# Optimization experiments

Hardware: AMD Instinct MI355X
Metric: run time of the kernel (lower is better)

## Reference

```python
import jax, jax.numpy as jnp
import numpy as np

NUM_TILES = 64
TPC = 8            # tiles per cluster
GRID = 16          # spline grid size
EPS = 1e-5


def setup_inputs() -> dict:
    key = jax.random.key(0)
    ks = jax.random.split(key, 6)
    B, S, D, T, DH, G = 2, 1024, 512, NUM_TILES, 128, GRID
    x = jax.random.normal(ks[0], (B, S, D), dtype=jnp.float32)
    gamma = jnp.ones((D,), jnp.float32)
    beta = jnp.zeros((D,), jnp.float32)
    # torch layouts: down.weight [DH, D], up.weight [D, DH]
    Wd = jax.random.normal(ks[1], (T, DH, D), dtype=jnp.float32) * 0.02
    spline_bases = jax.random.normal(ks[2], (T, DH, G), dtype=jnp.float32) * 0.1
    spline_slopes = jax.random.normal(ks[3], (T, DH, G), dtype=jnp.float32) * 0.1
    Wu = jax.random.normal(ks[4], (T, D, DH), dtype=jnp.float32) * 0.02
    scale = jnp.full((T,), 0.1, jnp.float32)
    return {"x": x, "gamma": gamma, "beta": beta, "Wd": Wd,
            "spline_bases": spline_bases, "spline_slopes": spline_slopes,
            "Wu": Wu, "scale": scale}


def reference(x, gamma, beta, Wd, spline_bases, spline_slopes, Wu, scale):
    B, S, D = x.shape
    T, DH, _ = Wd.shape
    C = T // TPC
    N = B * S

    # LayerNorm
    mu = x.mean(-1, keepdims=True)
    var = ((x - mu) ** 2).mean(-1, keepdims=True)
    xn = (x - mu) * jax.lax.rsqrt(var + EPS) * gamma + beta
    xf = xn.reshape(N, D)

    # Signatures (first call: ema == current tile signatures)
    tile_sigs = jnp.sign(Wd.mean(axis=1))                         # [T, D]
    cluster_sigs = jnp.sign(tile_sigs.reshape(C, TPC, D).mean(1))  # [C, D]

    # Hierarchical routing: cluster -> tile
    in_sigs = jnp.sign(xf)                                        # [N, D]
    best_c = jnp.argmax(in_sigs @ cluster_sigs.T, axis=-1)        # [N]
    tile_scores = (in_sigs @ tile_sigs.T).reshape(N, C, TPC)      # [N, C, TPC]
    sc = jnp.take_along_axis(tile_scores, best_c[:, None, None], axis=1)[:, 0, :]
    local_best = jnp.argmax(sc, axis=-1)                          # [N]
    tidx = best_c * TPC + local_best                              # [N]

    # Dispatch: gather per-token expert weights, down-project
    h = jnp.einsum('nd,nhd->nh', xf, Wd[tidx])                    # [N, DH]

    # Spline nonlinearity
    hn = jax.nn.sigmoid(h)
    idx = jnp.clip((hn * GRID).astype(jnp.int32), 0, GRID - 1)    # [N, DH]
    base = jnp.take_along_axis(spline_bases[tidx], idx[..., None], axis=-1)[..., 0]
    slope = jnp.take_along_axis(spline_slopes[tidx], idx[..., None], axis=-1)[..., 0]
    local_pos = hn * GRID - idx.astype(h.dtype)                   # (hn - idx*cell)/cell
    hs = base + slope * local_pos                                 # [N, DH]

    # Up-project, per-tile scale, combine (dropout is identity in eval)
    y = jnp.einsum('nh,ndh->nd', hs, Wu[tidx]) * scale[tidx][:, None]
    return x + y.reshape(B, S, D)
```

## Files before the change

### kernel.cpp

```cpp
#include <hip/hip_runtime.h>
#include <hip/hip_bf16.h>
#include <math.h>

#define NTILES 64
#define TPC 8
#define NCLUST 8
#define GRID_SZ 16
#define DIM 512
#define DHID 128
#define NTOK 2048
#define LN_EPS 1e-5f
#define TB 16
#define NCHUNK_MAX 192

typedef __attribute__((ext_vector_type(8))) short bf16x8;
typedef __attribute__((ext_vector_type(4))) float f32x4;

static __device__ __forceinline__ float fsign(float v) {
    return (v > 0.f) ? 1.f : ((v < 0.f) ? -1.f : 0.f);
}

static __device__ __forceinline__ unsigned short bf16bits(float f) {
    union { __hip_bfloat16 h; unsigned short s; } u;
    u.h = __float2bfloat16(f);
    return u.s;
}

static __device__ __forceinline__ bf16x8 cvt8(const float* p) {
    float4 a = *(const float4*)p;
    float4 b = *(const float4*)(p + 4);
    float e[8] = {a.x, a.y, a.z, a.w, b.x, b.y, b.z, b.w};
    bf16x8 v;
    #pragma unroll
    for (int i = 0; i < 8; ++i) v[i] = (short)bf16bits(e[i]);
    return v;
}

static __device__ __forceinline__ bool route_chunk(const int* counts, int lane, int cb,
                                                   int& t, int& base, int& m) {
    int cnt_l = counts[lane];
    int nck = (cnt_l + TB - 1) / TB;
    int pre = nck;
    #pragma unroll
    for (int off = 1; off < 64; off <<= 1) {
        int u = __shfl_up(pre, off);
        if (lane >= off) pre += u;
    }
    int total = __shfl(pre, 63);
    pre -= nck;
    if (cb >= total) return false;
    unsigned long long msk = __ballot(cb >= pre && cb < pre + nck);
    t = (int)__builtin_ctzll(msk);
    base = (cb - __shfl(pre, t)) * TB;
    m = min(TB, __shfl(cnt_l, t) - base);
    return true;
}

__global__ __launch_bounds__(256) void k_prep(const float* __restrict__ x,
                                              const float* __restrict__ gamma,
                                              const float* __restrict__ beta,
                                              const float* __restrict__ Wd,
                                              const float* __restrict__ Wu,
                                              float* __restrict__ psum,
                                              unsigned short* __restrict__ wd_b,
                                              unsigned short* __restrict__ wu_b,
                                              unsigned short* __restrict__ xn_b,
                                              int* __restrict__ counts) {
    int bid = blockIdx.x;
    int tid = threadIdx.x;
    if (bid < 512) {
        int t = bid >> 3, part = bid & 7;
        const float* basep = Wd + ((size_t)t * DHID + part * 16) * DIM;
        unsigned short* bb = wd_b + ((size_t)t * DHID + part * 16) * DIM;
        #pragma unroll
        for (int k2 = 0; k2 < 2; ++k2) {
            int d = tid + k2 * 256;
            float s = 0.f;
            #pragma unroll
            for (int j = 0; j < 16; ++j) {
                float v = basep[(size_t)j * DIM + d];
                s += v;
                bb[(size_t)j * DIM + d] = bf16bits(v);
            }
            psum[((size_t)t * 8 + part) * DIM + d] = s;
        }
        if (bid == 0 && tid < NTILES) counts[tid] = 0;
    } else if (bid < 1024) {
        int n = (bid - 512) * 4 + (tid >> 6);
        int lane = tid & 63;
        const float* xr = x + (size_t)n * DIM;
        float v[8];
        float sum = 0.f;
        #pragma unroll
        for (int j = 0; j < 8; ++j) { float t = xr[lane + 64 * j]; v[j] = t; sum += t; }
        #pragma unroll
        for (int off = 32; off; off >>= 1) sum += __shfl_xor(sum, off);
        float mu = sum * (1.f / DIM);
        float sq = 0.f;
        #pragma unroll
        for (int j = 0; j < 8; ++j) { float t = v[j] - mu; sq += t * t; }
        #pragma unroll
        for (int off = 32; off; off >>= 1) sq += __shfl_xor(sq, off);
        float rs = rsqrtf(sq * (1.f / DIM) + LN_EPS);
        #pragma unroll
        for (int j = 0; j < 8; ++j) {
            int d = lane + 64 * j;
            float xv = (v[j] - mu) * rs * gamma[d] + beta[d];
            xn_b[(size_t)n * DIM + d] = bf16bits(xv);
        }
    } else {
        size_t basei = (size_t)(bid - 1024) * 8192;
        #pragma unroll
        for (int k = 0; k < 4; ++k) {
            size_t off = basei + (size_t)tid * 8 + (size_t)k * 2048;
            bf16x8 v = cvt8(Wu + off);
            *(bf16x8*)(wu_b + off) = v;
        }
    }
}

__global__ __launch_bounds__(512) void k_csig(const float* __restrict__ psum,
                                              float* __restrict__ tile_sigs,
                                              float* __restrict__ cluster_sigs) {
    int c = blockIdx.x, d = threadIdx.x;
    float csum = 0.f;
    #pragma unroll
    for (int k = 0; k < TPC; ++k) {
        int t = c * TPC + k;
        float s = 0.f;
        #pragma unroll
        for (int p = 0; p < 8; ++p) s += psum[((size_t)t * 8 + p) * DIM + d];
        float sg = fsign(s);
        tile_sigs[(size_t)t * DIM + d] = sg;
        csum += sg;
    }
    cluster_sigs[(size_t)c * DIM + d] = fsign(csum);
}

__global__ __launch_bounds__(256) void k_route(const unsigned short* __restrict__ xn_b,
                                               const float* __restrict__ tile_sigs,
                                               const float* __restrict__ cluster_sigs,
                                               int* __restrict__ counts,
                                               int* __restrict__ list) {
    int n = blockIdx.x * 4 + (threadIdx.x >> 6);
    int lane = threadIdx.x & 63;
    float sg[8];
    #pragma unroll
    for (int j = 0; j < 8; ++j) {
        unsigned short u = xn_b[(size_t)n * DIM + lane + 64 * j];
        sg[j] = ((u & 0x7fff) == 0) ? 0.f : ((u & 0x8000) ? -1.f : 1.f);
    }
    int best_c = 0; float best = -1e30f;
    for (int c = 0; c < NCLUST; ++c) {
        float s = 0.f;
        #pragma unroll
        for (int j = 0; j < 8; ++j) s += sg[j] * cluster_sigs[(size_t)c * DIM + lane + 64 * j];
        #pragma unroll
        for (int off = 32; off; off >>= 1) s += __shfl_xor(s, off);
        if (s > best) { best = s; best_c = c; }
    }
    int bt = best_c * TPC; float bts = -1e30f;
    for (int k = 0; k < TPC; ++k) {
        int t = best_c * TPC + k;
        float s = 0.f;
        #pragma unroll
        for (int j = 0; j < 8; ++j) s += sg[j] * tile_sigs[(size_t)t * DIM + lane + 64 * j];
        #pragma unroll
        for (int off = 32; off; off >>= 1) s += __shfl_xor(s, off);
        if (s > bts) { bts = s; bt = t; }
    }
    if (lane == 0) {
        int slot = atomicAdd(&counts[bt], 1);
        list[(size_t)bt * NTOK + slot] = n;
    }
}

__global__ __launch_bounds__(512, 2) void k_ffn(const float* __restrict__ x,
                                                const unsigned short* __restrict__ xn_b,
                                                const unsigned short* __restrict__ wd_b,
                                                const float* __restrict__ sb,
                                                const float* __restrict__ ss,
                                                const unsigned short* __restrict__ wu_b,
                                                const float* __restrict__ scale,
                                                const int* __restrict__ counts,
                                                const int* __restrict__ list,
                                                float* __restrict__ out) {
    int tid = threadIdx.x;
    int lane = tid & 63;
    int wv = tid >> 6;
    int cb = ((int)blockIdx.x & 7) * (NCHUNK_MAX / 8) + ((int)blockIdx.x >> 3);
    int t, base, m;
    if (!route_chunk(counts, lane, cb, t, base, m)) return;

    __shared__ __align__(16) unsigned short hsl[TB * DHID];

    int mrow = lane & 15;
    int ko = (lane >> 4) * 8;
    int tokm = list[(size_t)t * NTOK + base + min(mrow, m - 1)];

    const unsigned short* xr = xn_b + (size_t)tokm * DIM;
    const unsigned short* wr = wd_b + ((size_t)t * DHID + wv * 16 + mrow) * DIM;
    f32x4 acc = {0.f, 0.f, 0.f, 0.f};
    #pragma unroll
    for (int kk = 0; kk < 16; ++kk) {
        int d = kk * 32 + ko;
        bf16x8 a = *(const bf16x8*)(xr + d);
        bf16x8 b = *(const bf16x8*)(wr + d);
        acc = __builtin_amdgcn_mfma_f32_16x16x32_bf16(a, b, acc, 0, 0, 0);
    }
    int dh = wv * 16 + mrow;
    const float* sbt = sb + ((size_t)t * DHID + dh) * GRID_SZ;
    const float* sst = ss + ((size_t)t * DHID + dh) * GRID_SZ;
    #pragma unroll
    for (int r = 0; r < 4; ++r) {
        int tr = (lane >> 4) * 4 + r;
        float h = acc[r];
        float hn = 1.f / (1.f + expf(-h));
        float g = hn * (float)GRID_SZ;
        int idx = (int)g;
        idx = idx > GRID_SZ - 1 ? GRID_SZ - 1 : idx;
        float lp = g - (float)idx;
        float val = sbt[idx] + sst[idx] * lp;
        hsl[(tr * DHID + dh) ^ ((tr & 7) << 3)] = bf16bits(val);
    }
    __syncthreads();

    float sc_t = scale[t];
    bf16x8 a2[4];
    #pragma unroll
    for (int kk = 0; kk < 4; ++kk)
        a2[kk] = *(const bf16x8*)&hsl[(mrow * DHID + kk * 32 + ko) ^ ((mrow & 7) << 3)];
    #pragma unroll
    for (int nt = 0; nt < 4; ++nt) {
        int d = wv * 64 + nt * 16 + mrow;
        const unsigned short* wru = wu_b + ((size_t)t * DIM + d) * DHID;
        f32x4 au = {0.f, 0.f, 0.f, 0.f};
        #pragma unroll
        for (int kk = 0; kk < 4; ++kk) {
            bf16x8 b = *(const bf16x8*)(wru + kk * 32 + ko);
            au = __builtin_amdgcn_mfma_f32_16x16x32_bf16(a2[kk], b, au, 0, 0, 0);
        }
        #pragma unroll
        for (int r = 0; r < 4; ++r) {
            int tr = (lane >> 4) * 4 + r;
            int tok_tr = __shfl(tokm, tr);
            if (tr < m) {
                size_t o = (size_t)tok_tr * DIM + d;
                out[o] = x[o] + au[r] * sc_t;
            }
        }
    }
}

extern "C" void kernel_launch(void* const* d_in, const int* in_sizes, int n_in,
                              void* d_out, int out_size, void* d_ws, size_t ws_size,
                              hipStream_t stream) {
    const float* x     = (const float*)d_in[0];
    const float* gamma = (const float*)d_in[1];
    const float* beta  = (const float*)d_in[2];
    const float* Wd    = (const float*)d_in[3];
    const float* sb    = (const float*)d_in[4];
    const float* ss    = (const float*)d_in[5];
    const float* Wu    = (const float*)d_in[6];
    const float* scale = (const float*)d_in[7];
    float* out = (float*)d_out;

    float* psum          = (float*)d_ws;
    float* tile_sigs     = psum + (size_t)NTILES * 8 * DIM;
    float* cluster_sigs  = tile_sigs + NTILES * DIM;
    int*   counts        = (int*)(cluster_sigs + NCLUST * DIM);
    int*   list          = counts + NTILES;
    unsigned short* xn_b = (unsigned short*)(list + (size_t)NTILES * NTOK);
    unsigned short* wd_b = xn_b + (size_t)NTOK * DIM;
    unsigned short* wu_b = wd_b + (size_t)NTILES * DHID * DIM;

    k_prep<<<1536, 256, 0, stream>>>(x, gamma, beta, Wd, Wu, psum, wd_b, wu_b, xn_b, counts);
    k_csig<<<NCLUST, 512, 0, stream>>>(psum, tile_sigs, cluster_sigs);
    k_route<<<NTOK / 4, 256, 0, stream>>>(xn_b, tile_sigs, cluster_sigs, counts, list);
    k_ffn<<<NCHUNK_MAX, 512, 0, stream>>>(x, xn_b, wd_b, sb, ss, wu_b, scale, counts, list, out);
}
```

Measured before the change: 51.94 us.

## Fuse four kernels into one persistent kernel with global atomic flag barriers

Replaces the prep, signature, routing and FFN launches with a single 1024-block kernel. Stages are ordered with global atomic counters and spin-waits instead of kernel boundaries, removing launch gaps and tail idle time. The FFN stage now uses 256-thread blocks that each cover two hidden and output slices per wave, and the Wu conversion is folded into the LayerNorm blocks. This depends on all 1024 blocks being co-resident, since otherwise the spin-waits deadlock, and it adds a memset and atomic polling traffic.

```diff
diff --git a/kernel.cpp b/kernel.cpp
--- a/kernel.cpp
+++ b/kernel.cpp
@@ -12,6 +12,12 @@
 #define LN_EPS 1e-5f
 #define TB 16
 #define NCHUNK_MAX 192
+#define NBLK 1024
+
+#define FA1 0
+#define FA2 16
+#define FB  32
+#define FC  48
 
 typedef __attribute__((ext_vector_type(8))) short bf16x8;
 typedef __attribute__((ext_vector_type(4))) float f32x4;
@@ -36,40 +42,35 @@
     return v;
 }
 
-static __device__ __forceinline__ bool route_chunk(const int* counts, int lane, int cb,
-                                                   int& t, int& base, int& m) {
-    int cnt_l = counts[lane];
-    int nck = (cnt_l + TB - 1) / TB;
-    int pre = nck;
-    #pragma unroll
-    for (int off = 1; off < 64; off <<= 1) {
-        int u = __shfl_up(pre, off);
-        if (lane >= off) pre += u;
-    }
-    int total = __shfl(pre, 63);
-    pre -= nck;
-    if (cb >= total) return false;
-    unsigned long long msk = __ballot(cb >= pre && cb < pre + nck);
-    t = (int)__builtin_ctzll(msk);
-    base = (cb - __shfl(pre, t)) * TB;
-    m = min(TB, __shfl(cnt_l, t) - base);
-    return true;
-}
-
-__global__ __launch_bounds__(256) void k_prep(const float* __restrict__ x,
-                                              const float* __restrict__ gamma,
-                                              const float* __restrict__ beta,
-                                              const float* __restrict__ Wd,
-                                              const float* __restrict__ Wu,
-                                              float* __restrict__ psum,
-                                              unsigned short* __restrict__ wd_b,
-                                              unsigned short* __restrict__ wu_b,
-                                              unsigned short* __restrict__ xn_b,
-                                              int* __restrict__ counts) {
-    int bid = blockIdx.x;
+static __device__ __forceinline__ void wait_flag(int* f, int target) {
+    while (atomicAdd(f, 0) < target) __builtin_amdgcn_s_sleep(8);
+}
+
+__global__ __launch_bounds__(256, 4) void k_all(const float* __restrict__ x,
+                                                const float* __restrict__ gamma,
+                                                const float* __restrict__ beta,
+                                                const float* __restrict__ Wd,
+                                                const float* __restrict__ sb,
+                                                const float* __restrict__ ss,
+                                                const float* __restrict__ Wu,
+                                                const float* __restrict__ scale,
+                                                float* __restrict__ out,
+                                                int* __restrict__ flags,
+                                                float* __restrict__ psum,
+                                                float* __restrict__ tile_sigs,
+                                                float* __restrict__ cluster_sigs,
+                                                int* __restrict__ counts,
+                                                int* __restrict__ list,
+                                                unsigned short* __restrict__ xn_b,
+                                                unsigned short* __restrict__ wd_b,
+                                                unsigned short* __restrict__ wu_b) {
+    int b = blockIdx.x;
     int tid = threadIdx.x;
-    if (bid < 512) {
-        int t = bid >> 3, part = bid & 7;
+    int lane = tid & 63;
+    int wv = tid >> 6;
+
+    if (b < 512) {
+        int t = b >> 3, part = b & 7;
         const float* basep = Wd + ((size_t)t * DHID + part * 16) * DIM;
         unsigned short* bb = wd_b + ((size_t)t * DHID + part * 16) * DIM;
         #pragma unroll
@@ -84,10 +85,8 @@
             }
             psum[((size_t)t * 8 + part) * DIM + d] = s;
         }
-        if (bid == 0 && tid < NTILES) counts[tid] = 0;
-    } else if (bid < 1024) {
-        int n = (bid - 512) * 4 + (tid >> 6);
-        int lane = tid & 63;
+    } else {
+        int n = (b - 512) * 4 + wv;
         const float* xr = x + (size_t)n * DIM;
         float v[8];
         float sum = 0.f;
@@ -108,120 +107,143 @@
             float xv = (v[j] - mu) * rs * gamma[d] + beta[d];
             xn_b[(size_t)n * DIM + d] = bf16bits(xv);
         }
-    } else {
-        size_t basei = (size_t)(bid - 1024) * 8192;
+        size_t basei = (size_t)(b - 512) * 8192;
         #pragma unroll
         for (int k = 0; k < 4; ++k) {
             size_t off = basei + (size_t)tid * 8 + (size_t)k * 2048;
-            bf16x8 v = cvt8(Wu + off);
-            *(bf16x8*)(wu_b + off) = v;
-        }
-    }
-}
-
-__global__ __launch_bounds__(512) void k_csig(const float* __restrict__ psum,
-                                              float* __restrict__ tile_sigs,
-                                              float* __restrict__ cluster_sigs) {
-    int c = blockIdx.x, d = threadIdx.x;
-    float csum = 0.f;
-    #pragma unroll
-    for (int k = 0; k < TPC; ++k) {
-        int t = c * TPC + k;
-        float s = 0.f;
-        #pragma unroll
-        for (int p = 0; p < 8; ++p) s += psum[((size_t)t * 8 + p) * DIM + d];
-        float sg = fsign(s);
-        tile_sigs[(size_t)t * DIM + d] = sg;
-        csum += sg;
-    }
-    cluster_sigs[(size_t)c * DIM + d] = fsign(csum);
-}
-
-__global__ __launch_bounds__(256) void k_route(const unsigned short* __restrict__ xn_b,
-                                               const float* __restrict__ tile_sigs,
-                                               const float* __restrict__ cluster_sigs,
-                                               int* __restrict__ counts,
-                                               int* __restrict__ list) {
-    int n = blockIdx.x * 4 + (threadIdx.x >> 6);
-    int lane = threadIdx.x & 63;
-    float sg[8];
-    #pragma unroll
-    for (int j = 0; j < 8; ++j) {
-        unsigned short u = xn_b[(size_t)n * DIM + lane + 64 * j];
-        sg[j] = ((u & 0x7fff) == 0) ? 0.f : ((u & 0x8000) ? -1.f : 1.f);
-    }
-    int best_c = 0; float best = -1e30f;
-    for (int c = 0; c < NCLUST; ++c) {
-        float s = 0.f;
-        #pragma unroll
-        for (int j = 0; j < 8; ++j) s += sg[j] * cluster_sigs[(size_t)c * DIM + lane + 64 * j];
-        #pragma unroll
-        for (int off = 32; off; off >>= 1) s += __shfl_xor(s, off);
-        if (s > best) { best = s; best_c = c; }
-    }
-    int bt = best_c * TPC; float bts = -1e30f;
-    for (int k = 0; k < TPC; ++k) {
-        int t = best_c * TPC + k;
-        float s = 0.f;
-        #pragma unroll
-        for (int j = 0; j < 8; ++j) s += sg[j] * tile_sigs[(size_t)t * DIM + lane + 64 * j];
-        #pragma unroll
-        for (int off = 32; off; off >>= 1) s += __shfl_xor(s, off);
-        if (s > bts) { bts = s; bt = t; }
-    }
-    if (lane == 0) {
-        int slot = atomicAdd(&counts[bt], 1);
-        list[(size_t)bt * NTOK + slot] = n;
-    }
-}
-
-__global__ __launch_bounds__(512, 2) void k_ffn(const float* __restrict__ x,
-                                                const unsigned short* __restrict__ xn_b,
-                                                const unsigned short* __restrict__ wd_b,
-                                                const float* __restrict__ sb,
-                                                const float* __restrict__ ss,
-                                                const unsigned short* __restrict__ wu_b,
-                                                const float* __restrict__ scale,
-                                                const int* __restrict__ counts,
-                                                const int* __restrict__ list,
-                                                float* __restrict__ out) {
-    int tid = threadIdx.x;
-    int lane = tid & 63;
-    int wv = tid >> 6;
-    int cb = ((int)blockIdx.x & 7) * (NCHUNK_MAX / 8) + ((int)blockIdx.x >> 3);
+            *(bf16x8*)(wu_b + off) = cvt8(Wu + off);
+        }
+    }
+    __syncthreads();
+    if (tid == 0) {
+        __threadfence();
+        atomicAdd(&flags[b < 512 ? FA1 : FA2], 1);
+    }
+    if (b >= 512) return;
+
+    if (b < NCLUST) {
+        if (tid == 0) { wait_flag(&flags[FA1], 512); __threadfence(); }
+        __syncthreads();
+        if (tid < TPC) counts[b * TPC + tid] = 0;
+        #pragma unroll
+        for (int k2 = 0; k2 < 2; ++k2) {
+            int d = tid + k2 * 256;
+            float csum = 0.f;
+            #pragma unroll
+            for (int k = 0; k < TPC; ++k) {
+                int t = b * TPC + k;
+                float s = 0.f;
+                #pragma unroll
+                for (int p = 0; p < 8; ++p) s += psum[((size_t)t * 8 + p) * DIM + d];
+                float sg = fsign(s);
+                tile_sigs[(size_t)t * DIM + d] = sg;
+                csum += sg;
+            }
+            cluster_sigs[(size_t)b * DIM + d] = fsign(csum);
+        }
+        __syncthreads();
+        if (tid == 0) { __threadfence(); atomicAdd(&flags[FB], 1); }
+    }
+
+    if (tid == 0) {
+        wait_flag(&flags[FB], NCLUST);
+        wait_flag(&flags[FA2], 512);
+        __threadfence();
+    }
+    __syncthreads();
+    {
+        int n = b * 4 + wv;
+        float sg[8];
+        #pragma unroll
+        for (int j = 0; j < 8; ++j) {
+            unsigned short u = xn_b[(size_t)n * DIM + lane + 64 * j];
+            sg[j] = ((u & 0x7fff) == 0) ? 0.f : ((u & 0x8000) ? -1.f : 1.f);
+        }
+        int best_c = 0; float best = -1e30f;
+        for (int c = 0; c < NCLUST; ++c) {
+            float s = 0.f;
+            #pragma unroll
+            for (int j = 0; j < 8; ++j) s += sg[j] * cluster_sigs[(size_t)c * DIM + lane + 64 * j];
+            #pragma unroll
+            for (int off = 32; off; off >>= 1) s += __shfl_xor(s, off);
+            if (s > best) { best = s; best_c = c; }
+        }
+        int bt = best_c * TPC; float bts = -1e30f;
+        for (int k = 0; k < TPC; ++k) {
+            int t = best_c * TPC + k;
+            float s = 0.f;
+            #pragma unroll
+            for (int j = 0; j < 8; ++j) s += sg[j] * tile_sigs[(size_t)t * DIM + lane + 64 * j];
+            #pragma unroll
+            for (int off = 32; off; off >>= 1) s += __shfl_xor(s, off);
+            if (s > bts) { bts = s; bt = t; }
+        }
+        if (lane == 0) {
+            int slot = atomicAdd(&counts[bt], 1);
+            list[(size_t)bt * NTOK + slot] = n;
+        }
+    }
+    __syncthreads();
+    if (tid == 0) { __threadfence(); atomicAdd(&flags[FC], 1); }
+    if (b >= NCHUNK_MAX) return;
+
+    if (tid == 0) { wait_flag(&flags[FC], 512); __threadfence(); }
+    __syncthreads();
+
+    int cb = (b & 7) * (NCHUNK_MAX / 8) + (b >> 3);
     int t, base, m;
-    if (!route_chunk(counts, lane, cb, t, base, m)) return;
+    {
+        int cnt_l = atomicAdd(&counts[lane], 0);
+        int nck = (cnt_l + TB - 1) / TB;
+        int pre = nck;
+        #pragma unroll
+        for (int off = 1; off < 64; off <<= 1) {
+            int u = __shfl_up(pre, off);
+            if (lane >= off) pre += u;
+        }
+        int total = __shfl(pre, 63);
+        pre -= nck;
+        if (cb >= total) return;
+        unsigned long long msk = __ballot(cb >= pre && cb < pre + nck);
+        t = (int)__builtin_ctzll(msk);
+        base = (cb - __shfl(pre, t)) * TB;
+        m = min(TB, __shfl(cnt_l, t) - base);
+    }
 
     __shared__ __align__(16) unsigned short hsl[TB * DHID];
 
     int mrow = lane & 15;
     int ko = (lane >> 4) * 8;
     int tokm = list[(size_t)t * NTOK + base + min(mrow, m - 1)];
-
     const unsigned short* xr = xn_b + (size_t)tokm * DIM;
-    const unsigned short* wr = wd_b + ((size_t)t * DHID + wv * 16 + mrow) * DIM;
-    f32x4 acc = {0.f, 0.f, 0.f, 0.f};
+
     #pragma unroll
-    for (int kk = 0; kk < 16; ++kk) {
-        int d = kk * 32 + ko;
-        bf16x8 a = *(const bf16x8*)(xr + d);
-        bf16x8 b = *(const bf16x8*)(wr + d);
-        acc = __builtin_amdgcn_mfma_f32_16x16x32_bf16(a, b, acc, 0, 0, 0);
-    }
-    int dh = wv * 16 + mrow;
-    const float* sbt = sb + ((size_t)t * DHID + dh) * GRID_SZ;
-    const float* sst = ss + ((size_t)t * DHID + dh) * GRID_SZ;
-    #pragma unroll
-    for (int r = 0; r < 4; ++r) {
-        int tr = (lane >> 4) * 4 + r;
-        float h = acc[r];
-        float hn = 1.f / (1.f + expf(-h));
-        float g = hn * (float)GRID_SZ;
-        int idx = (int)g;
-        idx = idx > GRID_SZ - 1 ? GRID_SZ - 1 : idx;
-        float lp = g - (float)idx;
-        float val = sbt[idx] + sst[idx] * lp;
-        hsl[(tr * DHID + dh) ^ ((tr & 7) << 3)] = bf16bits(val);
+    for (int j = 0; j < 2; ++j) {
+        int dtile = wv + j * 4;
+        const unsigned short* wr = wd_b + ((size_t)t * DHID + dtile * 16 + mrow) * DIM;
+        f32x4 acc = {0.f, 0.f, 0.f, 0.f};
+        #pragma unroll
+        for (int kk = 0; kk < 16; ++kk) {
+            int d = kk * 32 + ko;
+            bf16x8 a = *(const bf16x8*)(xr + d);
+            bf16x8 w = *(const bf16x8*)(wr + d);
+            acc = __builtin_amdgcn_mfma_f32_16x16x32_bf16(a, w, acc, 0, 0, 0);
+        }
+        int dh = dtile * 16 + mrow;
+        const float* sbt = sb + ((size_t)t * DHID + dh) * GRID_SZ;
+        const float* sst = ss + ((size_t)t * DHID + dh) * GRID_SZ;
+        #pragma unroll
+        for (int r = 0; r < 4; ++r) {
+            int tr = (lane >> 4) * 4 + r;
+            float h = acc[r];
+            float hn = 1.f / (1.f + expf(-h));
+            float g = hn * (float)GRID_SZ;
+            int idx = (int)g;
+            idx = idx > GRID_SZ - 1 ? GRID_SZ - 1 : idx;
+            float lp = g - (float)idx;
+            float val = sbt[idx] + sst[idx] * lp;
+            hsl[(tr * DHID + dh) ^ ((tr & 7) << 3)] = bf16bits(val);
+        }
     }
     __syncthreads();
 
@@ -231,22 +253,26 @@
     for (int kk = 0; kk < 4; ++kk)
         a2[kk] = *(const bf16x8*)&hsl[(mrow * DHID + kk * 32 + ko) ^ ((mrow & 7) << 3)];
     #pragma unroll
-    for (int nt = 0; nt < 4; ++nt) {
-        int d = wv * 64 + nt * 16 + mrow;
-        const unsigned short* wru = wu_b + ((size_t)t * DIM + d) * DHID;
-        f32x4 au = {0.f, 0.f, 0.f, 0.f};
-        #pragma unroll
-        for (int kk = 0; kk < 4; ++kk) {
-            bf16x8 b = *(const bf16x8*)(wru + kk * 32 + ko);
-            au = __builtin_amdgcn_mfma_f32_16x16x32_bf16(a2[kk], b, au, 0, 0, 0);
-        }
-        #pragma unroll
-        for (int r = 0; r < 4; ++r) {
-            int tr = (lane >> 4) * 4 + r;
-            int tok_tr = __shfl(tokm, tr);
-            if (tr < m) {
-                size_t o = (size_t)tok_tr * DIM + d;
-                out[o] = x[o] + au[r] * sc_t;
+    for (int j = 0; j < 2; ++j) {
+        int sl = wv + j * 4;
+        #pragma unroll
+        for (int nt = 0; nt < 4; ++nt) {
+            int d = sl * 64 + nt * 16 + mrow;
+            const unsigned short* wru = wu_b + ((size_t)t * DIM + d) * DHID;
+            f32x4 au = {0.f, 0.f, 0.f, 0.f};
+            #pragma unroll
+            for (int kk = 0; kk < 4; ++kk) {
+                bf16x8 w = *(const bf16x8*)(wru + kk * 32 + ko);
+                au = __builtin_amdgcn_mfma_f32_16x16x32_bf16(a2[kk], w, au, 0, 0, 0);
+            }
+            #pragma unroll
+            for (int r = 0; r < 4; ++r) {
+                int tr = (lane >> 4) * 4 + r;
+                int tok_tr = __shfl(tokm, tr);
+                if (tr < m) {
+                    size_t o = (size_t)tok_tr * DIM + d;
+                    out[o] = x[o] + au[r] * sc_t;
+                }
             }
         }
     }
@@ -265,7 +291,8 @@
     const float* scale = (const float*)d_in[7];
     float* out = (float*)d_out;
 
-    float* psum          = (float*)d_ws;
+    int*   flags         = (int*)d_ws;
+    float* psum          = (float*)((char*)d_ws + 256);
     float* tile_sigs     = psum + (size_t)NTILES * 8 * DIM;
     float* cluster_sigs  = tile_sigs + NTILES * DIM;
     int*   counts        = (int*)(cluster_sigs + NCLUST * DIM);
@@ -274,8 +301,8 @@
     unsigned short* wd_b = xn_b + (size_t)NTOK * DIM;
     unsigned short* wu_b = wd_b + (size_t)NTILES * DHID * DIM;
 
-    k_prep<<<1536, 256, 0, stream>>>(x, gamma, beta, Wd, Wu, psum, wd_b, wu_b, xn_b, counts);
-    k_csig<<<NCLUST, 512, 0, stream>>>(psum, tile_sigs, cluster_sigs);
-    k_route<<<NTOK / 4, 256, 0, stream>>>(xn_b, tile_sigs, cluster_sigs, counts, list);
-    k_ffn<<<NCHUNK_MAX, 512, 0, stream>>>(x, xn_b, wd_b, sb, ss, wu_b, scale, counts, list, out);
-}
+    hipMemsetAsync(flags, 0, 256, stream);
+    k_all<<<NBLK, 256, 0, stream>>>(x, gamma, beta, Wd, sb, ss, Wu, scale, out,
+                                    flags, psum, tile_sigs, cluster_sigs,
+                                    counts, list, xn_b, wd_b, wu_b);
+}
```

New measurement: 129.9 us. 2.5x slower.
